# Optimization experiments

Hardware: AMD Instinct MI355X
Metric: run time of the kernel (lower is better)

## Reference

```python
import jax, jax.numpy as jnp
import numpy as np

N, E, IN, H, ED = 50000, 800000, 128, 128, 3
EPS = 1e-5

def _gat_conv(x, src, dst, ea, W, a_src, a_dst, We, a_edge, bias):
    n = x.shape[0]
    # add self loops; self-loop edge_attr = per-feature mean (PyG fill_value='mean')
    loops = jnp.arange(n, dtype=src.dtype)
    s = jnp.concatenate([src, loops])
    d = jnp.concatenate([dst, loops])
    ea_full = jnp.concatenate([ea, jnp.broadcast_to(ea.mean(0), (n, ea.shape[1]))], 0)
    h = x @ W                       # [n, H]
    al_s = h @ a_src                # [n]
    al_d = h @ a_dst
    al_e = (ea_full @ We) @ a_edge  # [E+n]
    alpha = jax.nn.leaky_relu(al_s[s] + al_d[d] + al_e, 0.2)
    # segment softmax over destination nodes (every node has a self loop)
    amax = jax.ops.segment_max(alpha, d, num_segments=n)
    ex = jnp.exp(alpha - amax[d])
    denom = jax.ops.segment_sum(ex, d, num_segments=n)
    coef = ex / (denom[d] + 1e-16)
    out = jax.ops.segment_sum(h[s] * coef[:, None], d, num_segments=n)
    return out + bias

def _bn(x, gamma, beta):
    mu = x.mean(0)
    var = ((x - mu) ** 2).mean(0)
    return (x - mu) * jax.lax.rsqrt(var + EPS) * gamma + beta

def setup_inputs():
    key = jax.random.key(0)
    ks = jax.random.split(key, 40)
    inp = {
        "x": jax.random.normal(ks[0], (N, IN), jnp.float32),
        "edge_index": jax.random.randint(ks[1], (2, E), 0, N, dtype=jnp.int32),
        "batch": jnp.zeros((N,), jnp.int32),
        "edge_attr": jax.random.normal(ks[2], (E, ED), jnp.float32),
    }
    i = 3
    for l, cin in ((1, IN), (2, H), (3, H)):
        s = 1.0 / np.sqrt(cin)
        inp[f"W{l}"] = jax.random.normal(ks[i], (cin, H), jnp.float32) * s; i += 1
        inp[f"as{l}"] = jax.random.normal(ks[i], (H,), jnp.float32) * 0.1; i += 1
        inp[f"ad{l}"] = jax.random.normal(ks[i], (H,), jnp.float32) * 0.1; i += 1
        inp[f"We{l}"] = jax.random.normal(ks[i], (ED, H), jnp.float32) * 0.5; i += 1
        inp[f"ae{l}"] = jax.random.normal(ks[i], (H,), jnp.float32) * 0.1; i += 1
        inp[f"b{l}"] = jnp.zeros((H,), jnp.float32)
        inp[f"g{l}"] = jnp.ones((H,), jnp.float32)
        inp[f"be{l}"] = jnp.zeros((H,), jnp.float32)
    return inp

def reference(x, edge_index, batch, edge_attr,
              W1, as1, ad1, We1, ae1, b1, g1, be1,
              W2, as2, ad2, We2, ae2, b2, g2, be2,
              W3, as3, ad3, We3, ae3, b3, g3, be3):
    src, dst = edge_index[0], edge_index[1]
    h = _gat_conv(x, src, dst, edge_attr, W1, as1, ad1, We1, ae1, b1)
    h = _bn(jax.nn.leaky_relu(h, 0.01), g1, be1)
    h = _gat_conv(h, src, dst, edge_attr, W2, as2, ad2, We2, ae2, b2)
    h = _bn(jax.nn.leaky_relu(h, 0.01), g2, be2)
    h = _gat_conv(h, src, dst, edge_attr, W3, as3, ad3, We3, ae3, b3)
    h = _bn(jax.nn.leaky_relu(h, 0.01), g3, be3)
    return h
```

## Files before the change

kernel.cpp:

```cpp
#include <hip/hip_runtime.h>
#include <math.h>


struct __align__(16) Edge { int src; float e0, e1, e2; };

__device__ __forceinline__ unsigned short f2bf(float x) {
  unsigned u = __float_as_uint(x);
  unsigned r = (u + 0x7FFFu + ((u >> 16) & 1u)) >> 16;
  return (unsigned short)r;
}

__global__ void k_hist(const int* __restrict__ dst, int E, int* __restrict__ deg) {
  int i = blockIdx.x * blockDim.x + threadIdx.x;
  if (i < E) atomicAdd(&deg[dst[i]], 1);
}

__global__ void k_ea_sum(const float* __restrict__ ea, int E, float* __restrict__ ea_sum) {
  float s0 = 0.f, s1 = 0.f, s2 = 0.f;
  for (int i = blockIdx.x * blockDim.x + threadIdx.x; i < E; i += gridDim.x * blockDim.x) {
    s0 += ea[i * 3 + 0]; s1 += ea[i * 3 + 1]; s2 += ea[i * 3 + 2];
  }
  for (int off = 32; off; off >>= 1) {
    s0 += __shfl_down(s0, off); s1 += __shfl_down(s1, off); s2 += __shfl_down(s2, off);
  }
  __shared__ float ls[3][4];
  int lane = threadIdx.x & 63, w = threadIdx.x >> 6;
  if (lane == 0) { ls[0][w] = s0; ls[1][w] = s1; ls[2][w] = s2; }
  __syncthreads();
  if (threadIdx.x == 0) {
    float t0 = 0.f, t1 = 0.f, t2 = 0.f;
    for (int ww = 0; ww < 4; ++ww) { t0 += ls[0][ww]; t1 += ls[1][ww]; t2 += ls[2][ww]; }
    atomicAdd(&ea_sum[0], t0); atomicAdd(&ea_sum[1], t1); atomicAdd(&ea_sum[2], t2);
  }
}

__device__ __forceinline__ int wave_incl_scan(int x, int lane) {
  for (int off = 1; off < 64; off <<= 1) {
    int t = __shfl_up(x, off);
    if (lane >= off) x += t;
  }
  return x;
}

__global__ __launch_bounds__(1024) void k_scan_a(const int* __restrict__ deg, int n,
                                                 int* __restrict__ start,
                                                 int* __restrict__ bsum) {
  __shared__ int wsum[16];
  int t = threadIdx.x, lane = t & 63, w = t >> 6;
  int i = blockIdx.x * 1024 + t;
  int v = (i < n) ? deg[i] : 0;
  int x = wave_incl_scan(v, lane);
  if (lane == 63) wsum[w] = x;
  __syncthreads();
  if (w == 0 && lane < 16) {
    int s = wsum[lane];
    for (int off = 1; off < 16; off <<= 1) {
      int u = __shfl_up(s, off);
      if (lane >= off) s += u;
    }
    wsum[lane] = s;
  }
  __syncthreads();
  int woff = w ? wsum[w - 1] : 0;
  if (i < n) start[i] = x - v + woff;
  if (t == 1023) bsum[blockIdx.x] = wsum[15];
}

__global__ void k_scan_b(int* __restrict__ bsum, int nb, int* __restrict__ start, int n) {
  int lane = threadIdx.x;
  int v = (lane < nb) ? bsum[lane] : 0;
  int x = wave_incl_scan(v, lane);
  if (lane < nb) bsum[lane] = x - v;
  if (lane == nb - 1) start[n] = x;
}

__global__ void k_scan_c(int* __restrict__ start, const int* __restrict__ bsum, int n,
                         int* __restrict__ cursor) {
  int i = blockIdx.x * blockDim.x + threadIdx.x;
  if (i < n) {
    int s = start[i] + bsum[i >> 10];
    start[i] = s;
    cursor[i] = s;
  }
}

__global__ void k_scatter(const int* __restrict__ src, const int* __restrict__ dst,
                          const float* __restrict__ ea, int E,
                          int* __restrict__ cursor, Edge* __restrict__ edges,
                          int* __restrict__ srcs, int* __restrict__ dsts) {
  int i = blockIdx.x * blockDim.x + threadIdx.x;
  if (i >= E) return;
  int d = dst[i];
  int pos = atomicAdd(&cursor[d], 1);
  Edge e;
  int s = src[i];
  e.src = s;
  e.e0 = ea[i * 3 + 0]; e.e1 = ea[i * 3 + 1]; e.e2 = ea[i * 3 + 2];
  edges[pos] = e;
  srcs[pos] = s;
  dsts[pos] = d;
}

__global__ void k_initid(float* __restrict__ sc, float* __restrict__ sh) {
  int c = threadIdx.x;
  sc[c] = 1.f; sh[c] = 0.f;
}

__global__ void k_param(const float* __restrict__ We, const float* __restrict__ ae,
                        const float* __restrict__ ea_sum, float invE, float* __restrict__ P) {
  int lane = threadIdx.x;
  float a0 = ae[lane], a1 = ae[64 + lane];
  float p0 = We[0 * 128 + lane] * a0 + We[0 * 128 + 64 + lane] * a1;
  float p1 = We[1 * 128 + lane] * a0 + We[1 * 128 + 64 + lane] * a1;
  float p2 = We[2 * 128 + lane] * a0 + We[2 * 128 + 64 + lane] * a1;
  for (int off = 32; off; off >>= 1) {
    p0 += __shfl_down(p0, off); p1 += __shfl_down(p1, off); p2 += __shfl_down(p2, off);
  }
  if (lane == 0) {
    P[0] = p0; P[1] = p1; P[2] = p2;
    P[3] = ea_sum[0] * invE * p0 + ea_sum[1] * invE * p1 + ea_sum[2] * invE * p2;
  }
}

__global__ __launch_bounds__(256) void k_gemm2(
    const float* __restrict__ X, const float* __restrict__ Wm,
    const float* __restrict__ bnsc, const float* __restrict__ bnsh,
    const float* __restrict__ as, const float* __restrict__ ad,
    const float* __restrict__ P,
    unsigned* __restrict__ hb, float* __restrict__ al_s, float* __restrict__ al_d,
    float* __restrict__ es, int n) {
  __shared__ float wl[128 * 128];
  __shared__ float xs[32 * 128];
  int t = threadIdx.x;
  for (int i = t; i < 4096; i += 256) ((float4*)wl)[i] = ((const float4*)Wm)[i];
  int c32 = t & 31;
  int c4 = c32 << 2;
  int rq = t >> 5;
  int lane = t & 63;
  float4 av_s = *(const float4*)(as + c4);
  float4 av_d = *(const float4*)(ad + c4);
  float cself = P[3];
  int ntiles = (n + 31) >> 5;
  for (int tile = blockIdx.x; tile < ntiles; tile += gridDim.x) {
    int r0 = tile << 5;
    __syncthreads();
    for (int i = t; i < 1024; i += 256) {
      int rr = i >> 5, cc = i & 31;
      int g = r0 + rr;
      float4 v;
      if (g < n) {
        v = ((const float4*)(X + (size_t)g * 128))[cc];
        float4 sc = ((const float4*)bnsc)[cc];
        float4 sh = ((const float4*)bnsh)[cc];
        v.x = fmaf(v.x, sc.x, sh.x); v.y = fmaf(v.y, sc.y, sh.y);
        v.z = fmaf(v.z, sc.z, sh.z); v.w = fmaf(v.w, sc.w, sh.w);
      } else { v.x = v.y = v.z = v.w = 0.f; }
      ((float4*)xs)[i] = v;
    }
    __syncthreads();
    float4 acc[4];
    for (int r = 0; r < 4; ++r) { acc[r].x = acc[r].y = acc[r].z = acc[r].w = 0.f; }
    const float* xr = xs + (rq << 2) * 128;
#pragma unroll 4
    for (int k = 0; k < 128; ++k) {
      float4 w4 = ((const float4*)wl)[(k << 5) + c32];
#pragma unroll
      for (int r = 0; r < 4; ++r) {
        float xv = xr[r * 128 + k];
        acc[r].x = fmaf(xv, w4.x, acc[r].x);
        acc[r].y = fmaf(xv, w4.y, acc[r].y);
        acc[r].z = fmaf(xv, w4.z, acc[r].z);
        acc[r].w = fmaf(xv, w4.w, acc[r].w);
      }
    }
    int gbase = r0 + (rq << 2);
#pragma unroll
    for (int r = 0; r < 4; ++r) {
      int g = gbase + r;
      float4 o = acc[r];
      if (g < n) {
        unsigned u01 = ((unsigned)f2bf(o.y) << 16) | (unsigned)f2bf(o.x);
        unsigned u23 = ((unsigned)f2bf(o.w) << 16) | (unsigned)f2bf(o.z);
        uint2 uu = {u01, u23};
        *(uint2*)(hb + (size_t)g * 64 + (c32 << 1)) = uu;
      }
      float ps = o.x * av_s.x + o.y * av_s.y + o.z * av_s.z + o.w * av_s.w;
      float pd = o.x * av_d.x + o.y * av_d.y + o.z * av_d.z + o.w * av_d.w;
      for (int off = 16; off; off >>= 1) {
        ps += __shfl_xor(ps, off);
        pd += __shfl_xor(pd, off);
      }
      if ((lane & 31) == 0 && g < n) {
        al_s[g] = ps; al_d[g] = pd;
        float a = ps + pd + cself;
        a = a > 0.f ? a : 0.2f * a;
        es[g] = __expf(a);
      }
    }
  }
}

__global__ __launch_bounds__(256) void k_alpha2(const float4* __restrict__ edges,
                                                const int* __restrict__ dsts,
                                                const float* __restrict__ al_s,
                                                const float* __restrict__ al_d,
                                                const float* __restrict__ P,
                                                float* __restrict__ pexp, int E) {
  int i = blockIdx.x * blockDim.x + threadIdx.x;
  if (i >= E) return;
  float4 ef = edges[i];
  int s = __float_as_int(ef.x);
  float a = al_s[s] + al_d[dsts[i]] + ef.y * P[0] + ef.z * P[1] + ef.w * P[2];
  a = a > 0.f ? a : 0.2f * a;
  pexp[i] = __expf(a);
}

__global__ __launch_bounds__(256) void k_agg4(const int* __restrict__ srcs,
                                              const float* __restrict__ pexp,
                                              const int* __restrict__ start,
                                              const unsigned* __restrict__ hb,
                                              const float* __restrict__ es,
                                              const float* __restrict__ bias,
                                              float* __restrict__ y,
                                              float* __restrict__ colsum,
                                              float* __restrict__ colsumsq, int n) {
  int lane = threadIdx.x & 63;
  int w = threadIdx.x >> 6;
  int gw = (blockIdx.x * blockDim.x + threadIdx.x) >> 6;
  int nw = (gridDim.x * blockDim.x) >> 6;
  float2 b2 = ((const float2*)bias)[lane];
  float s0 = 0.f, s1 = 0.f, q0 = 0.f, q1 = 0.f;
  for (int i = gw; i < n; i += nw) {
    int e0 = __builtin_amdgcn_readfirstlane(start[i]);
    int e1 = __builtin_amdgcn_readfirstlane(start[i + 1]);
    float eself = es[i];
    unsigned hv = hb[(size_t)i * 64 + lane];
    float hx = __uint_as_float(hv << 16);
    float hy = __uint_as_float(hv & 0xFFFF0000u);
    float aX0 = eself * hx, aY0 = eself * hy;
    float aX1 = 0.f, aY1 = 0.f, aX2 = 0.f, aY2 = 0.f, aX3 = 0.f, aY3 = 0.f;
    float pacc = 0.f;
    int e = e0;
    for (; e + 8 <= e1; e += 8) {
      int sv[8]; float pv[8]; unsigned gv[8];
#pragma unroll
      for (int k = 0; k < 8; ++k) sv[k] = srcs[e + k];
#pragma unroll
      for (int k = 0; k < 8; ++k) pv[k] = pexp[e + k];
#pragma unroll
      for (int k = 0; k < 8; ++k) gv[k] = hb[(size_t)sv[k] * 64 + lane];
#pragma unroll
      for (int k = 0; k < 8; ++k) {
        float gx = __uint_as_float(gv[k] << 16);
        float gy = __uint_as_float(gv[k] & 0xFFFF0000u);
        pacc += pv[k];
        if ((k & 3) == 0) { aX0 = fmaf(pv[k], gx, aX0); aY0 = fmaf(pv[k], gy, aY0); }
        else if ((k & 3) == 1) { aX1 = fmaf(pv[k], gx, aX1); aY1 = fmaf(pv[k], gy, aY1); }
        else if ((k & 3) == 2) { aX2 = fmaf(pv[k], gx, aX2); aY2 = fmaf(pv[k], gy, aY2); }
        else { aX3 = fmaf(pv[k], gx, aX3); aY3 = fmaf(pv[k], gy, aY3); }
      }
    }
    for (; e < e1; ++e) {
      int sv = srcs[e];
      float pv = pexp[e];
      unsigned gv = hb[(size_t)sv * 64 + lane];
      float gx = __uint_as_float(gv << 16);
      float gy = __uint_as_float(gv & 0xFFFF0000u);
      pacc += pv;
      aX0 = fmaf(pv, gx, aX0); aY0 = fmaf(pv, gy, aY0);
    }
    float inv = 1.0f / (eself + pacc + 1e-16f);
    float o0 = (aX0 + aX1) + (aX2 + aX3);
    float o1 = (aY0 + aY1) + (aY2 + aY3);
    o0 = fmaf(o0, inv, b2.x);
    o1 = fmaf(o1, inv, b2.y);
    o0 = o0 > 0.f ? o0 : 0.01f * o0;
    o1 = o1 > 0.f ? o1 : 0.01f * o1;
    float2 o2 = {o0, o1};
    ((float2*)(y + (size_t)i * 128))[lane] = o2;
    s0 += o0; s1 += o1;
    q0 = fmaf(o0, o0, q0); q1 = fmaf(o1, o1, q1);
  }
  __shared__ float red[4][4][64];
  red[0][w][lane] = s0; red[1][w][lane] = s1; red[2][w][lane] = q0; red[3][w][lane] = q1;
  __syncthreads();
  if (w == 0) {
    for (int ww = 1; ww < 4; ++ww) {
      s0 += red[0][ww][lane]; s1 += red[1][ww][lane];
      q0 += red[2][ww][lane]; q1 += red[3][ww][lane];
    }
    atomicAdd(&colsum[2 * lane], s0);
    atomicAdd(&colsum[2 * lane + 1], s1);
    atomicAdd(&colsumsq[2 * lane], q0);
    atomicAdd(&colsumsq[2 * lane + 1], q1);
  }
}

__global__ void k_bnfinal(const float* __restrict__ colsum, const float* __restrict__ colsumsq,
                          const float* __restrict__ g, const float* __restrict__ be,
                          float invN, float* __restrict__ scale, float* __restrict__ shift) {
  int c = threadIdx.x;
  float mu = colsum[c] * invN;
  float var = colsumsq[c] * invN - mu * mu;
  var = var > 0.f ? var : 0.f;
  float sc = g[c] * rsqrtf(var + 1e-5f);
  scale[c] = sc;
  shift[c] = be[c] - mu * sc;
}

__global__ void k_bnapply(const float4* __restrict__ yin, const float* __restrict__ scale,
                          const float* __restrict__ shift, float4* __restrict__ yout, int total4) {
  int i = blockIdx.x * blockDim.x + threadIdx.x;
  if (i >= total4) return;
  int c4 = i & 31;
  float4 v = yin[i];
  float4 sc = ((const float4*)scale)[c4];
  float4 sh = ((const float4*)shift)[c4];
  v.x = fmaf(v.x, sc.x, sh.x);
  v.y = fmaf(v.y, sc.y, sh.y);
  v.z = fmaf(v.z, sc.z, sh.z);
  v.w = fmaf(v.w, sc.w, sh.w);
  yout[i] = v;
}

extern "C" void kernel_launch(void* const* d_in, const int* in_sizes, int n_in,
                              void* d_out, int out_size, void* d_ws, size_t ws_size,
                              hipStream_t stream) {
  const float* x = (const float*)d_in[0];
  const int* eidx = (const int*)d_in[1];
  const float* ea = (const float*)d_in[3];
  const int H = 128;
  const int N = in_sizes[0] / H;
  const int E = in_sizes[1] / 2;
  const int* srcIdx = eidx;
  const int* dstIdx = eidx + E;

  char* ws = (char*)d_ws;
  size_t off = 0;
  auto alloc = [&](size_t bytes) -> void* {
    void* p = ws + off;
    off = (off + bytes + 255) & ~(size_t)255;
    return p;
  };
  Edge* edges = (Edge*)alloc((size_t)E * sizeof(Edge));
  int* srcs = (int*)alloc((size_t)E * sizeof(int));
  int* dsts = (int*)alloc((size_t)E * sizeof(int));
  float* pexp = (float*)alloc((size_t)E * sizeof(float));
  unsigned* hb = (unsigned*)alloc((size_t)N * 64 * sizeof(unsigned));
  float* y = (float*)alloc((size_t)N * H * sizeof(float));
  float* al_s = (float*)alloc((size_t)N * sizeof(float));
  float* al_d = (float*)alloc((size_t)N * sizeof(float));
  float* es = (float*)alloc((size_t)N * sizeof(float));
  int* deg = (int*)alloc((size_t)N * sizeof(int));
  int* start = (int*)alloc((size_t)(N + 1) * sizeof(int));
  int* cursor = (int*)alloc((size_t)N * sizeof(int));
  int* bsum = (int*)alloc(64 * sizeof(int));
  float* colsum = (float*)alloc(128 * sizeof(float));
  float* colsumsq = (float*)alloc(128 * sizeof(float));
  float* scale = (float*)alloc(128 * sizeof(float));
  float* shift = (float*)alloc(128 * sizeof(float));
  float* ea_sum = (float*)alloc(16 * sizeof(float));
  float* P = (float*)alloc(16 * sizeof(float));

  const int nb = (N + 1023) / 1024;

  hipMemsetAsync(deg, 0, (size_t)N * sizeof(int), stream);
  hipMemsetAsync(ea_sum, 0, 16 * sizeof(float), stream);
  k_hist<<<(E + 255) / 256, 256, 0, stream>>>(dstIdx, E, deg);
  k_ea_sum<<<256, 256, 0, stream>>>(ea, E, ea_sum);
  k_scan_a<<<nb, 1024, 0, stream>>>(deg, N, start, bsum);
  k_scan_b<<<1, 64, 0, stream>>>(bsum, nb, start, N);
  k_scan_c<<<(N + 255) / 256, 256, 0, stream>>>(start, bsum, N, cursor);
  k_scatter<<<(E + 255) / 256, 256, 0, stream>>>(srcIdx, dstIdx, ea, E, cursor, edges, srcs, dsts);
  k_initid<<<1, 128, 0, stream>>>(scale, shift);

  const float* X = x;
  for (int l = 0; l < 3; ++l) {
    const float* W = (const float*)d_in[4 + 8 * l + 0];
    const float* as = (const float*)d_in[4 + 8 * l + 1];
    const float* ad = (const float*)d_in[4 + 8 * l + 2];
    const float* We = (const float*)d_in[4 + 8 * l + 3];
    const float* ae = (const float*)d_in[4 + 8 * l + 4];
    const float* b = (const float*)d_in[4 + 8 * l + 5];
    const float* g = (const float*)d_in[4 + 8 * l + 6];
    const float* be = (const float*)d_in[4 + 8 * l + 7];

    hipMemsetAsync(colsum, 0, 128 * sizeof(float), stream);
    hipMemsetAsync(colsumsq, 0, 128 * sizeof(float), stream);
    k_param<<<1, 64, 0, stream>>>(We, ae, ea_sum, 1.0f / (float)E, P);
    k_gemm2<<<512, 256, 0, stream>>>(X, W, scale, shift, as, ad, P, hb, al_s, al_d, es, N);
    k_alpha2<<<(E + 255) / 256, 256, 0, stream>>>((const float4*)edges, dsts, al_s, al_d, P,
                                                  pexp, E);
    k_agg4<<<2048, 256, 0, stream>>>(srcs, pexp, start, hb, es, b, y, colsum, colsumsq, N);
    k_bnfinal<<<1, 128, 0, stream>>>(colsum, colsumsq, g, be, 1.0f / (float)N, scale, shift);
    X = y;
  }
  k_bnapply<<<((N * 32) + 255) / 256, 256, 0, stream>>>((const float4*)y, scale, shift,
                                                        (float4*)d_out, N * 32);
}
```

Measured before the change: 783.4 us.

## Pack src+exp into edge meta and split wave halves across edges in aggregation

The alpha kernel now writes a packed (src, exp) pair per edge, replacing the separate srcs and pexp arrays. The aggregation kernel loads up to 64 edges' metadata in one coalesced wave load and broadcasts it with shuffles. Each half-wave then gathers a different edge's bf16 row using 8-byte-per-lane loads, and the two halves are combined with a cross-half shuffle. This is meant to cut scalar index loads and double the number of gathers in flight per wave, at the cost of more shuffles and only half the lanes doing the final store and stats. The two column-stat memsets are also merged into one.

```diff
diff --git a/kernel.cpp b/kernel.cpp
--- a/kernel.cpp
+++ b/kernel.cpp
@@ -9,6 +9,8 @@
   unsigned r = (u + 0x7FFFu + ((u >> 16) & 1u)) >> 16;
   return (unsigned short)r;
 }
+__device__ __forceinline__ float bf_lo(unsigned u) { return __uint_as_float(u << 16); }
+__device__ __forceinline__ float bf_hi(unsigned u) { return __uint_as_float(u & 0xFFFF0000u); }
 
 __global__ void k_hist(const int* __restrict__ dst, int E, int* __restrict__ deg) {
   int i = blockIdx.x * blockDim.x + threadIdx.x;
@@ -87,17 +89,15 @@
 __global__ void k_scatter(const int* __restrict__ src, const int* __restrict__ dst,
                           const float* __restrict__ ea, int E,
                           int* __restrict__ cursor, Edge* __restrict__ edges,
-                          int* __restrict__ srcs, int* __restrict__ dsts) {
+                          int* __restrict__ dsts) {
   int i = blockIdx.x * blockDim.x + threadIdx.x;
   if (i >= E) return;
   int d = dst[i];
   int pos = atomicAdd(&cursor[d], 1);
   Edge e;
-  int s = src[i];
-  e.src = s;
+  e.src = src[i];
   e.e0 = ea[i * 3 + 0]; e.e1 = ea[i * 3 + 1]; e.e2 = ea[i * 3 + 2];
   edges[pos] = e;
-  srcs[pos] = s;
   dsts[pos] = d;
 }
 
@@ -200,25 +200,25 @@
   }
 }
 
-__global__ __launch_bounds__(256) void k_alpha2(const float4* __restrict__ edges,
+__global__ __launch_bounds__(256) void k_alpha3(const float4* __restrict__ edges,
                                                 const int* __restrict__ dsts,
                                                 const float* __restrict__ al_s,
                                                 const float* __restrict__ al_d,
                                                 const float* __restrict__ P,
-                                                float* __restrict__ pexp, int E) {
+                                                uint2* __restrict__ meta, int E) {
   int i = blockIdx.x * blockDim.x + threadIdx.x;
   if (i >= E) return;
   float4 ef = edges[i];
   int s = __float_as_int(ef.x);
   float a = al_s[s] + al_d[dsts[i]] + ef.y * P[0] + ef.z * P[1] + ef.w * P[2];
   a = a > 0.f ? a : 0.2f * a;
-  pexp[i] = __expf(a);
-}
-
-__global__ __launch_bounds__(256) void k_agg4(const int* __restrict__ srcs,
-                                              const float* __restrict__ pexp,
+  uint2 m = {(unsigned)s, __float_as_uint(__expf(a))};
+  meta[i] = m;
+}
+
+__global__ __launch_bounds__(256) void k_agg5(const uint2* __restrict__ meta,
                                               const int* __restrict__ start,
-                                              const unsigned* __restrict__ hb,
+                                              const uint2* __restrict__ hb2,
                                               const float* __restrict__ es,
                                               const float* __restrict__ bias,
                                               float* __restrict__ y,
@@ -226,73 +226,91 @@
                                               float* __restrict__ colsumsq, int n) {
   int lane = threadIdx.x & 63;
   int w = threadIdx.x >> 6;
+  int half = lane >> 5;
+  int hl = lane & 31;
   int gw = (blockIdx.x * blockDim.x + threadIdx.x) >> 6;
   int nw = (gridDim.x * blockDim.x) >> 6;
-  float2 b2 = ((const float2*)bias)[lane];
-  float s0 = 0.f, s1 = 0.f, q0 = 0.f, q1 = 0.f;
+  float4 b4 = ((const float4*)bias)[hl];
+  float s0 = 0.f, s1 = 0.f, s2 = 0.f, s3 = 0.f;
+  float q0 = 0.f, q1 = 0.f, q2 = 0.f, q3 = 0.f;
   for (int i = gw; i < n; i += nw) {
-    int e0 = __builtin_amdgcn_readfirstlane(start[i]);
-    int e1 = __builtin_amdgcn_readfirstlane(start[i + 1]);
+    int e0 = start[i];
+    int e1 = start[i + 1];
     float eself = es[i];
-    unsigned hv = hb[(size_t)i * 64 + lane];
-    float hx = __uint_as_float(hv << 16);
-    float hy = __uint_as_float(hv & 0xFFFF0000u);
-    float aX0 = eself * hx, aY0 = eself * hy;
-    float aX1 = 0.f, aY1 = 0.f, aX2 = 0.f, aY2 = 0.f, aX3 = 0.f, aY3 = 0.f;
-    float pacc = 0.f;
-    int e = e0;
-    for (; e + 8 <= e1; e += 8) {
-      int sv[8]; float pv[8]; unsigned gv[8];
+    uint2 sv = hb2[(size_t)i * 32 + hl];
+    float pself = (half == 0) ? eself : 0.f;
+    float a0 = pself * bf_lo(sv.x), a1 = pself * bf_hi(sv.x);
+    float a2 = pself * bf_lo(sv.y), a3 = pself * bf_hi(sv.y);
+    float pacc = pself;
+    for (int wb = e0; wb < e1; wb += 64) {
+      int wcount = e1 - wb; if (wcount > 64) wcount = 64;
+      uint2 m;
+      if (lane < wcount) m = meta[wb + lane];
+      else { m.x = 0u; m.y = 0u; }
+      int mx = (int)m.x;
+      float mp = __uint_as_float(m.y);
+      int rounds = (wcount + 15) >> 4;
+      for (int r = 0; r < rounds; ++r) {
+        int gb = r << 3;
+        int sl[8]; float pl[8]; uint2 gv[8];
 #pragma unroll
-      for (int k = 0; k < 8; ++k) sv[k] = srcs[e + k];
+        for (int k = 0; k < 8; ++k) {
+          int srcLane = ((gb + k) << 1) + half;
+          sl[k] = __shfl(mx, srcLane);
+          pl[k] = __shfl(mp, srcLane);
+        }
 #pragma unroll
-      for (int k = 0; k < 8; ++k) pv[k] = pexp[e + k];
+        for (int k = 0; k < 8; ++k) gv[k] = hb2[(size_t)sl[k] * 32 + hl];
 #pragma unroll
-      for (int k = 0; k < 8; ++k) gv[k] = hb[(size_t)sv[k] * 64 + lane];
-#pragma unroll
-      for (int k = 0; k < 8; ++k) {
-        float gx = __uint_as_float(gv[k] << 16);
-        float gy = __uint_as_float(gv[k] & 0xFFFF0000u);
-        pacc += pv[k];
-        if ((k & 3) == 0) { aX0 = fmaf(pv[k], gx, aX0); aY0 = fmaf(pv[k], gy, aY0); }
-        else if ((k & 3) == 1) { aX1 = fmaf(pv[k], gx, aX1); aY1 = fmaf(pv[k], gy, aY1); }
-        else if ((k & 3) == 2) { aX2 = fmaf(pv[k], gx, aX2); aY2 = fmaf(pv[k], gy, aY2); }
-        else { aX3 = fmaf(pv[k], gx, aX3); aY3 = fmaf(pv[k], gy, aY3); }
+        for (int k = 0; k < 8; ++k) {
+          float pk = pl[k];
+          pacc += pk;
+          a0 = fmaf(pk, bf_lo(gv[k].x), a0);
+          a1 = fmaf(pk, bf_hi(gv[k].x), a1);
+          a2 = fmaf(pk, bf_lo(gv[k].y), a2);
+          a3 = fmaf(pk, bf_hi(gv[k].y), a3);
+        }
       }
     }
-    for (; e < e1; ++e) {
-      int sv = srcs[e];
-      float pv = pexp[e];
-      unsigned gv = hb[(size_t)sv * 64 + lane];
-      float gx = __uint_as_float(gv << 16);
-      float gy = __uint_as_float(gv & 0xFFFF0000u);
-      pacc += pv;
-      aX0 = fmaf(pv, gx, aX0); aY0 = fmaf(pv, gy, aY0);
-    }
-    float inv = 1.0f / (eself + pacc + 1e-16f);
-    float o0 = (aX0 + aX1) + (aX2 + aX3);
-    float o1 = (aY0 + aY1) + (aY2 + aY3);
-    o0 = fmaf(o0, inv, b2.x);
-    o1 = fmaf(o1, inv, b2.y);
+    a0 += __shfl_xor(a0, 32); a1 += __shfl_xor(a1, 32);
+    a2 += __shfl_xor(a2, 32); a3 += __shfl_xor(a3, 32);
+    pacc += __shfl_xor(pacc, 32);
+    float inv = 1.0f / (pacc + 1e-16f);
+    float o0 = fmaf(a0, inv, b4.x);
+    float o1 = fmaf(a1, inv, b4.y);
+    float o2 = fmaf(a2, inv, b4.z);
+    float o3 = fmaf(a3, inv, b4.w);
     o0 = o0 > 0.f ? o0 : 0.01f * o0;
     o1 = o1 > 0.f ? o1 : 0.01f * o1;
-    float2 o2 = {o0, o1};
-    ((float2*)(y + (size_t)i * 128))[lane] = o2;
-    s0 += o0; s1 += o1;
-    q0 = fmaf(o0, o0, q0); q1 = fmaf(o1, o1, q1);
-  }
-  __shared__ float red[4][4][64];
-  red[0][w][lane] = s0; red[1][w][lane] = s1; red[2][w][lane] = q0; red[3][w][lane] = q1;
+    o2 = o2 > 0.f ? o2 : 0.01f * o2;
+    o3 = o3 > 0.f ? o3 : 0.01f * o3;
+    if (half == 0) {
+      float4 ov = {o0, o1, o2, o3};
+      *(float4*)(y + (size_t)i * 128 + (hl << 2)) = ov;
+      s0 += o0; s1 += o1; s2 += o2; s3 += o3;
+      q0 = fmaf(o0, o0, q0); q1 = fmaf(o1, o1, q1);
+      q2 = fmaf(o2, o2, q2); q3 = fmaf(o3, o3, q3);
+    }
+  }
+  __shared__ float redS[4][32][4];
+  __shared__ float redQ[4][32][4];
+  if (half == 0) {
+    redS[w][hl][0] = s0; redS[w][hl][1] = s1; redS[w][hl][2] = s2; redS[w][hl][3] = s3;
+    redQ[w][hl][0] = q0; redQ[w][hl][1] = q1; redQ[w][hl][2] = q2; redQ[w][hl][3] = q3;
+  }
   __syncthreads();
-  if (w == 0) {
+  if (w == 0 && half == 0) {
     for (int ww = 1; ww < 4; ++ww) {
-      s0 += red[0][ww][lane]; s1 += red[1][ww][lane];
-      q0 += red[2][ww][lane]; q1 += red[3][ww][lane];
-    }
-    atomicAdd(&colsum[2 * lane], s0);
-    atomicAdd(&colsum[2 * lane + 1], s1);
-    atomicAdd(&colsumsq[2 * lane], q0);
-    atomicAdd(&colsumsq[2 * lane + 1], q1);
+      s0 += redS[ww][hl][0]; s1 += redS[ww][hl][1];
+      s2 += redS[ww][hl][2]; s3 += redS[ww][hl][3];
+      q0 += redQ[ww][hl][0]; q1 += redQ[ww][hl][1];
+      q2 += redQ[ww][hl][2]; q3 += redQ[ww][hl][3];
+    }
+    int f = hl << 2;
+    atomicAdd(&colsum[f + 0], s0); atomicAdd(&colsum[f + 1], s1);
+    atomicAdd(&colsum[f + 2], s2); atomicAdd(&colsum[f + 3], s3);
+    atomicAdd(&colsumsq[f + 0], q0); atomicAdd(&colsumsq[f + 1], q1);
+    atomicAdd(&colsumsq[f + 2], q2); atomicAdd(&colsumsq[f + 3], q3);
   }
 }
 
@@ -343,9 +361,8 @@
     return p;
   };
   Edge* edges = (Edge*)alloc((size_t)E * sizeof(Edge));
-  int* srcs = (int*)alloc((size_t)E * sizeof(int));
   int* dsts = (int*)alloc((size_t)E * sizeof(int));
-  float* pexp = (float*)alloc((size_t)E * sizeof(float));
+  uint2* meta = (uint2*)alloc((size_t)E * sizeof(uint2));
   unsigned* hb = (unsigned*)alloc((size_t)N * 64 * sizeof(unsigned));
   float* y = (float*)alloc((size_t)N * H * sizeof(float));
   float* al_s = (float*)alloc((size_t)N * sizeof(float));
@@ -355,8 +372,9 @@
   int* start = (int*)alloc((size_t)(N + 1) * sizeof(int));
   int* cursor = (int*)alloc((size_t)N * sizeof(int));
   int* bsum = (int*)alloc(64 * sizeof(int));
-  float* colsum = (float*)alloc(128 * sizeof(float));
-  float* colsumsq = (float*)alloc(128 * sizeof(float));
+  float* colstats = (float*)alloc(256 * sizeof(float));
+  float* colsum = colstats;
+  float* colsumsq = colstats + 128;
   float* scale = (float*)alloc(128 * sizeof(float));
   float* shift = (float*)alloc(128 * sizeof(float));
   float* ea_sum = (float*)alloc(16 * sizeof(float));
@@ -371,7 +389,7 @@
   k_scan_a<<<nb, 1024, 0, stream>>>(deg, N, start, bsum);
   k_scan_b<<<1, 64, 0, stream>>>(bsum, nb, start, N);
   k_scan_c<<<(N + 255) / 256, 256, 0, stream>>>(start, bsum, N, cursor);
-  k_scatter<<<(E + 255) / 256, 256, 0, stream>>>(srcIdx, dstIdx, ea, E, cursor, edges, srcs, dsts);
+  k_scatter<<<(E + 255) / 256, 256, 0, stream>>>(srcIdx, dstIdx, ea, E, cursor, edges, dsts);
   k_initid<<<1, 128, 0, stream>>>(scale, shift);
 
   const float* X = x;
@@ -385,13 +403,13 @@
     const float* g = (const float*)d_in[4 + 8 * l + 6];
     const float* be = (const float*)d_in[4 + 8 * l + 7];
 
-    hipMemsetAsync(colsum, 0, 128 * sizeof(float), stream);
-    hipMemsetAsync(colsumsq, 0, 128 * sizeof(float), stream);
+    hipMemsetAsync(colstats, 0, 256 * sizeof(float), stream);
     k_param<<<1, 64, 0, stream>>>(We, ae, ea_sum, 1.0f / (float)E, P);
     k_gemm2<<<512, 256, 0, stream>>>(X, W, scale, shift, as, ad, P, hb, al_s, al_d, es, N);
-    k_alpha2<<<(E + 255) / 256, 256, 0, stream>>>((const float4*)edges, dsts, al_s, al_d, P,
-                                                  pexp, E);
-    k_agg4<<<2048, 256, 0, stream>>>(srcs, pexp, start, hb, es, b, y, colsum, colsumsq, N);
+    k_alpha3<<<(E + 255) / 256, 256, 0, stream>>>((const float4*)edges, dsts, al_s, al_d, P,
+                                                  meta, E);
+    k_agg5<<<2048, 256, 0, stream>>>(meta, start, (const uint2*)hb, es, b, y,
+                                     colsum, colsumsq, N);
     k_bnfinal<<<1, 128, 0, stream>>>(colsum, colsumsq, g, be, 1.0f / (float)N, scale, shift);
     X = y;
   }
```

Result: slower. 1.052 ms (+34.3%).
